# Kernel optimization log

Hardware: AMD Instinct MI355X
Metric: run time of the kernel (lower is better)

Reference implementation:

```python
import jax, jax.numpy as jnp
import numpy as np

K = 16  # neighbors


def _knn_indices(coords, k):
    # coords: (B, 3, N) -> indices (B, N, k) of k nearest points (incl. self)
    sq = jnp.sum(coords * coords, axis=1)                      # (B, N)
    d2 = sq[:, :, None] + sq[:, None, :] - 2.0 * jnp.einsum('bcn,bcm->bnm', coords, coords)
    _, idx = jax.lax.top_k(-d2, k)                             # smallest distances
    return idx


def _gather(points, idx):
    # points: (B, C, N), idx: (B, N, k) -> (B, C, N, k)
    return jax.vmap(lambda p, i: p[:, i])(points, idx)


def setup_inputs() -> dict:
    key = jax.random.key(0)
    ks = jax.random.split(key, 8)
    B, N, C_IN, C_OUT = 4, 8192, 64, 64
    s = 0.05
    return {
        'features': jax.random.normal(ks[0], (B, C_IN, N), dtype=jnp.float32),
        'coords': jax.random.normal(ks[1], (B, 3, N), dtype=jnp.float32),
        'w_lin': jax.random.normal(ks[2], (3 * C_OUT, C_IN), dtype=jnp.float32) * s,
        'w_theta1': jax.random.normal(ks[3], (C_OUT, 3), dtype=jnp.float32) * s,
        'w_theta2': jax.random.normal(ks[4], (C_OUT, C_OUT), dtype=jnp.float32) * s,
        'w_gamma1': jax.random.normal(ks[5], (C_OUT, C_OUT), dtype=jnp.float32) * s,
        'w_gamma2': jax.random.normal(ks[6], (C_OUT, C_OUT), dtype=jnp.float32) * s,
    }


def reference(features, coords, w_lin, w_theta1, w_theta2, w_gamma1, w_gamma2):
    # KNN (int indices, non-differentiable)
    idx = _knn_indices(coords, K)                              # (B, N, k)

    knn_coords = _gather(coords, idx)                          # (B, 3, N, k)
    rel = coords[:, :, :, None] - knn_coords                   # localize * -1
    delta = jnp.einsum('oc,bcnk->bonk', w_theta1, rel)
    delta = jax.nn.relu(jnp.einsum('oc,bcnk->bonk', w_theta2, delta))  # (B, Co, N, k)

    # input linear -> phi, psi, alpha
    feat3 = jnp.einsum('oc,bcn->bon', w_lin, features)         # (B, 3*Co, N)
    phi, psi, alpha = jnp.split(feat3, 3, axis=1)

    psi_g = _gather(psi, idx)                                  # (B, Co, N, k)
    inputs_gamma = phi[:, :, :, None] - psi_g + delta          # localize*-1 + delta
    g = jnp.einsum('oc,bcnk->bonk', w_gamma1, inputs_gamma)
    g = jax.nn.relu(jnp.einsum('oc,bcnk->bonk', w_gamma2, g))
    rho = jax.nn.softmax(g, axis=-1)                           # softmax over k

    alpha_g = _gather(alpha, idx) + delta                      # (B, Co, N, k)
    return jnp.sum(rho * alpha_g, axis=-1)                     # (B, Co, N)
```

## Files before the change

kernel.cpp:

```cpp
#include <hip/hip_runtime.h>
#include <cstdint>


#define NPT 8192
typedef unsigned long long u64;
typedef unsigned int u32;
typedef unsigned short u16;
typedef __attribute__((ext_vector_type(8))) short bf8_t;
typedef __attribute__((ext_vector_type(4))) float f32x4;

__device__ __forceinline__ u16 f2bf(float x) {
  return (u16)((__float_as_uint(x) + 0x8000u) >> 16);
}
__device__ __forceinline__ u32 pkbf(float lo, float hi) {
  return (u32)f2bf(lo) | ((u32)f2bf(hi) << 16);
}
__device__ __forceinline__ float bf2f(u16 v) {
  return __uint_as_float((u32)v << 16);
}
__device__ __forceinline__ u32 med3u(u32 a, u32 b, u32 c) {
  u32 d;
  asm("v_med3_u32 %0, %1, %2, %3" : "=v"(d) : "v"(a), "v"(b), "v"(c));
  return d;
}
__device__ __forceinline__ u32 wave_min_u32(u32 v) {
  u32 t;
  t = (u32)__builtin_amdgcn_update_dpp((int)v, (int)v, 0x111, 0xF, 0xF, false); v = min(v, t);
  t = (u32)__builtin_amdgcn_update_dpp((int)v, (int)v, 0x112, 0xF, 0xF, false); v = min(v, t);
  t = (u32)__builtin_amdgcn_update_dpp((int)v, (int)v, 0x114, 0xF, 0xF, false); v = min(v, t);
  t = (u32)__builtin_amdgcn_update_dpp((int)v, (int)v, 0x118, 0xF, 0xF, false); v = min(v, t);
  t = (u32)__builtin_amdgcn_update_dpp((int)v, (int)v, 0x142, 0xF, 0xF, false); v = min(v, t);
  t = (u32)__builtin_amdgcn_update_dpp((int)v, (int)v, 0x143, 0xF, 0xF, false); v = min(v, t);
  return (u32)__builtin_amdgcn_readlane((int)v, 63);
}
__device__ __forceinline__ u32 wave_max_u32(u32 v) {
  u32 t;
  t = (u32)__builtin_amdgcn_update_dpp((int)v, (int)v, 0x111, 0xF, 0xF, false); v = max(v, t);
  t = (u32)__builtin_amdgcn_update_dpp((int)v, (int)v, 0x112, 0xF, 0xF, false); v = max(v, t);
  t = (u32)__builtin_amdgcn_update_dpp((int)v, (int)v, 0x114, 0xF, 0xF, false); v = max(v, t);
  t = (u32)__builtin_amdgcn_update_dpp((int)v, (int)v, 0x118, 0xF, 0xF, false); v = max(v, t);
  t = (u32)__builtin_amdgcn_update_dpp((int)v, (int)v, 0x142, 0xF, 0xF, false); v = max(v, t);
  t = (u32)__builtin_amdgcn_update_dpp((int)v, (int)v, 0x143, 0xF, 0xF, false); v = max(v, t);
  return (u32)__builtin_amdgcn_readlane((int)v, 63);
}
__device__ __forceinline__ void lds_cp16(float4* lds_dst, const float4* gsrc) {
  __builtin_amdgcn_global_load_lds(
      (const __attribute__((address_space(1))) unsigned int*)(const void*)gsrc,
      (__attribute__((address_space(3))) unsigned int*)(void*)lds_dst, 16, 0, 0);
}

__global__ __launch_bounds__(256) void fold1_k(
    const float* __restrict__ wg1, const float* __restrict__ wg2,
    const float* __restrict__ wt1, const float* __restrict__ wt2,
    float* __restrict__ G, float* __restrict__ Mrow, float* __restrict__ McT) {
  int t = blockIdx.x * 256 + threadIdx.x;
  if (t < 4096) {
    int o = t >> 6, c = t & 63;
    float acc = 0.f;
    for (int cp = 0; cp < 64; ++cp) acc = fmaf(wg2[o * 64 + cp], wg1[cp * 64 + c], acc);
    G[o * 64 + c] = acc;
  } else if (t < 4096 + 192) {
    int i = t - 4096;
    int o = i / 3, j = i - o * 3;
    float acc = 0.f;
    for (int c = 0; c < 64; ++c) acc = fmaf(wt2[o * 64 + c], wt1[c * 3 + j], acc);
    Mrow[o * 3 + j] = acc;
    McT[j * 64 + o] = acc;
  }
}

__global__ __launch_bounds__(256) void fold2_k(
    const float* __restrict__ G, const float* __restrict__ wl,
    u16* __restrict__ GF, u16* __restrict__ WF) {
  int t = blockIdx.x * 256 + threadIdx.x;
  if (t < 12288) {
    int o = t >> 6, c = t & 63;
    float acc = 0.f;
    if (o < 64) {
      for (int cp = 0; cp < 64; ++cp) acc = fmaf(G[o * 64 + cp], wl[cp * 64 + c], acc);
    } else if (o < 128) {
      for (int cp = 0; cp < 64; ++cp) acc = fmaf(G[(o - 64) * 64 + cp], wl[(64 + cp) * 64 + c], acc);
    } else {
      acc = wl[o * 64 + c];
    }
    int ot = o >> 4, m = o & 15;
    int kh = c >> 5, q = (c >> 3) & 3, j = c & 7;
    WF[(((ot * 2 + kh) * 64) + (q * 16 + m)) * 8 + j] = f2bf(acc);
  } else {
    int i = t - 12288;
    int o = i >> 6, c = i & 63;
    int ot = o >> 4, m = o & 15;
    int kh = c >> 5, q = (c >> 3) & 3, j = c & 7;
    GF[(((ot * 2 + kh) * 64) + (q * 16 + m)) * 8 + j] = f2bf(G[o * 64 + c]);
  }
}

__global__ __launch_bounds__(256) void pack_k(const float* __restrict__ coords,
                                              float4* __restrict__ pack) {
  int g = blockIdx.x * 256 + threadIdx.x;
  int b = g >> 13, n = g & (NPT - 1);
  const float* c = coords + (size_t)b * 3 * NPT;
  float x = c[n], y = c[NPT + n], z = c[2 * NPT + n];
  float sq = __fadd_rn(__fadd_rn(__fmul_rn(x, x), __fmul_rn(y, y)), __fmul_rn(z, z));
  pack[g] = make_float4(x, y, z, sq);
}

#define QPB 8
#define CHUNK 1024
#define NQ 32768
__global__ __launch_bounds__(512) void knn_k(const float4* __restrict__ pack,
                                             u32* __restrict__ part) {
  __shared__ float4 C[2][CHUNK];
  int tid = threadIdx.x;
  int w = tid >> 6, lane = tid & 63;
  int query = blockIdx.x * QPB + w;
  int b = query >> 13, n = query & (NPT - 1);
  const float4* pk = pack + (size_t)b * NPT;
  float4 q = pk[n];
  float qsq = q.w;
  u32 arr[8];
#pragma unroll
  for (int j = 0; j < 8; ++j) arr[j] = 0xFFFFFFFFu;
  lds_cp16(&C[0][tid], pk + tid);
  lds_cp16(&C[0][512 + tid], pk + 512 + tid);
  __syncthreads();
  u32 tau = 0xFFFFFFFFu;
  for (int c0 = 0; c0 < NPT; c0 += CHUNK) {
    int cur = (c0 >> 10) & 1;
    if (c0 + CHUNK < NPT) {
      lds_cp16(&C[cur ^ 1][tid], pk + (c0 + CHUNK) + tid);
      lds_cp16(&C[cur ^ 1][512 + tid], pk + (c0 + CHUNK) + 512 + tid);
    }
#pragma unroll 4
    for (int t = 0; t < CHUNK / 64; ++t) {
      float4 c4 = C[cur][t * 64 + lane];
      float dot = fmaf(q.z, c4.z, fmaf(q.y, c4.y, q.x * c4.x));
      float d2 = fmaxf(fmaf(-2.f, dot, qsq + c4.w), 0.f);
      u32 key = (__float_as_uint(d2) & 0xFFFFE000u) | (u32)(c0 + t * 64 + lane);
      if (key < min(arr[7], tau)) {
        arr[7] = med3u(key, arr[6], arr[7]);
        arr[6] = med3u(key, arr[5], arr[6]);
        arr[5] = med3u(key, arr[4], arr[5]);
        arr[4] = med3u(key, arr[3], arr[4]);
        arr[3] = med3u(key, arr[2], arr[3]);
        arr[2] = med3u(key, arr[1], arr[2]);
        arr[1] = med3u(key, arr[0], arr[1]);
        arr[0] = min(arr[0], key);
      }
    }
    tau = wave_max_u32(arr[0]);
    __syncthreads();
  }
  u32 mg = 0xFFFFFFFFu;
#pragma unroll 1
  for (int r = 0; r < 24; ++r) {
    u32 m = wave_min_u32(arr[0]);
    if (lane == r) mg = m;
    if (arr[0] == m) {
      arr[0] = arr[1]; arr[1] = arr[2]; arr[2] = arr[3]; arr[3] = arr[4];
      arr[4] = arr[5]; arr[5] = arr[6]; arr[6] = arr[7]; arr[7] = 0xFFFFFFFFu;
    }
  }
  if (lane < 24) part[(size_t)lane * NQ + query] = mg;
}

__global__ __launch_bounds__(64) void refine_k(const float4* __restrict__ pack,
                                               const u32* __restrict__ part,
                                               int* __restrict__ idxk) {
  int g = blockIdx.x * 64 + threadIdx.x;
  int b = g >> 13;
  const float4* pk = pack + (size_t)b * NPT;
  float4 q = pk[g & (NPT - 1)];
  float qx = q.x, qy = q.y, qz = q.z, qs = q.w;
  float bd[16];
  int bi[16];
#pragma unroll
  for (int j = 0; j < 16; ++j) { bd[j] = 1e30f; bi[j] = 0x7FFFFFFF; }
#pragma unroll 4
  for (int j = 0; j < 24; ++j) {
    int m = (int)(part[(size_t)j * NQ + g] & 0x1FFFu);
    float4 pm = pk[m];
    float dot = __fadd_rn(__fadd_rn(__fmul_rn(qx, pm.x), __fmul_rn(qy, pm.y)),
                          __fmul_rn(qz, pm.z));
    float kd = __fsub_rn(__fadd_rn(qs, pm.w), __fmul_rn(2.0f, dot));
    int ki = m;
    if (kd < bd[15] || (kd == bd[15] && ki < bi[15])) {
#pragma unroll
      for (int qq = 0; qq < 16; ++qq) {
        bool cs = (kd < bd[qq]) || (kd == bd[qq] && ki < bi[qq]);
        float td = bd[qq];
        int ti = bi[qq];
        bd[qq] = cs ? kd : td;
        bi[qq] = cs ? ki : ti;
        kd = cs ? td : kd;
        ki = cs ? ti : ki;
      }
    }
  }
#pragma unroll
  for (int j = 0; j < 16; ++j) idxk[(size_t)g * 16 + j] = bi[j];
}

__global__ __launch_bounds__(256) void feat_k(const float* __restrict__ features,
                                              const u16* __restrict__ WF,
                                              float* __restrict__ featA,
                                              u16* __restrict__ featB) {
  int tid = threadIdx.x;
  int w = tid >> 6, l = tid & 63;
  int quad = l >> 4, col = l & 15;
  int P = blockIdx.x * 64 + w * 16 + col;
  int b = P >> 13, n = P & (NPT - 1);
  const float* fb = features + (size_t)b * 64 * NPT + n;
  const bf8_t* wfr = (const bf8_t*)WF;
  bf8_t Bf[2];
#pragma unroll
  for (int kh = 0; kh < 2; ++kh) {
    union { u32 wv[4]; bf8_t v; } ub;
#pragma unroll
    for (int j2 = 0; j2 < 4; ++j2) {
      float lo = fb[(size_t)(kh * 32 + quad * 8 + j2 * 2) * NPT];
      float hi = fb[(size_t)(kh * 32 + quad * 8 + j2 * 2 + 1) * NPT];
      ub.wv[j2] = pkbf(lo, hi);
    }
    Bf[kh] = ub.v;
  }
#pragma unroll
  for (int ot = 0; ot < 12; ++ot) {
    bf8_t A0 = wfr[(ot * 2 + 0) * 64 + l];
    bf8_t A1 = wfr[(ot * 2 + 1) * 64 + l];
    f32x4 acc = {0.f, 0.f, 0.f, 0.f};
    acc = __builtin_amdgcn_mfma_f32_16x16x32_bf16(A0, Bf[0], acc, 0, 0, 0);
    acc = __builtin_amdgcn_mfma_f32_16x16x32_bf16(A1, Bf[1], acc, 0, 0, 0);
    int gr = ot * 16 + quad * 4;
    if (ot < 4) {
      *(float4*)(featA + (size_t)P * 64 + gr) = make_float4(acc[0], acc[1], acc[2], acc[3]);
    } else {
      uint2 wv2 = make_uint2(pkbf(acc[0], acc[1]), pkbf(acc[2], acc[3]));
      *(uint2*)(featB + (size_t)P * 128 + (gr - 64)) = wv2;
    }
  }
}

#define SROW 68
__global__ __launch_bounds__(64) void attn_k(
    const float4* __restrict__ pack, const int* __restrict__ idxk,
    const float* __restrict__ featA, const u16* __restrict__ featB,
    const u16* __restrict__ GF, const float* __restrict__ Mrow,
    const float* __restrict__ McT, float* __restrict__ out) {
  __shared__ u16 S16[64 * SROW];
  int l = threadIdx.x;
  int quad = l >> 4, col = l & 15;
  int Pb = blockIdx.x * 4;
  int b = Pb >> 13;
  int nb0 = Pb & (NPT - 1);
  const float4* pkb = pack + (size_t)b * NPT;
  int idxv = idxk[(size_t)Pb * 16 + l];
  int mve[4];
#pragma unroll
  for (int t = 0; t < 4; ++t) mve[t] = __shfl(idxv, t * 16 + col);
  float relx[4], rely[4], relz[4];
#pragma unroll
  for (int t = 0; t < 4; ++t) {
    float4 own = pkb[nb0 + t];
    float4 nbr = pkb[mve[t]];
    relx[t] = own.x - nbr.x; rely[t] = own.y - nbr.y; relz[t] = own.z - nbr.z;
  }
  bf8_t Bf[4][2];
#pragma unroll
  for (int kh = 0; kh < 2; ++kh) {
    const float* mr = Mrow + (kh * 32 + quad * 8) * 3;
    float m_[24];
#pragma unroll
    for (int i6 = 0; i6 < 6; ++i6) {
      float4 v = *(const float4*)(mr + i6 * 4);
      m_[i6 * 4] = v.x; m_[i6 * 4 + 1] = v.y; m_[i6 * 4 + 2] = v.z; m_[i6 * 4 + 3] = v.w;
    }
#pragma unroll
    for (int t = 0; t < 4; ++t) {
      float u_[8];
#pragma unroll
      for (int j = 0; j < 8; ++j)
        u_[j] = fmaxf(fmaf(m_[j * 3 + 2], relz[t],
                           fmaf(m_[j * 3 + 1], rely[t], m_[j * 3] * relx[t])), 0.f);
      union { u32 w[4]; bf8_t v; } ub;
#pragma unroll
      for (int j2 = 0; j2 < 4; ++j2) ub.w[j2] = pkbf(u_[j2 * 2], u_[j2 * 2 + 1]);
      Bf[t][kh] = ub.v;
    }
  }
  const bf8_t* gfr = (const bf8_t*)GF;
#pragma unroll
  for (int ot = 0; ot < 4; ++ot) {
    bf8_t A0 = gfr[(ot * 2 + 0) * 64 + l];
    bf8_t A1 = gfr[(ot * 2 + 1) * 64 + l];
#pragma unroll
    for (int pt = 0; pt < 4; ++pt) {
      f32x4 acc = {0.f, 0.f, 0.f, 0.f};
      acc = __builtin_amdgcn_mfma_f32_16x16x32_bf16(A0, Bf[pt][0], acc, 0, 0, 0);
      acc = __builtin_amdgcn_mfma_f32_16x16x32_bf16(A1, Bf[pt][1], acc, 0, 0, 0);
      const float* phn = featA + (size_t)(Pb + pt) * 64 + ot * 16 + quad * 4;
      float4 ph = *(const float4*)phn;
      uint2 psw = *(const uint2*)(featB + ((size_t)b * NPT + mve[pt]) * 128 + ot * 16 + quad * 4);
      float g0 = fmaxf(acc[0] + ph.x - bf2f((u16)(psw.x & 0xFFFF)), 0.f);
      float g1 = fmaxf(acc[1] + ph.y - bf2f((u16)(psw.x >> 16)), 0.f);
      float g2 = fmaxf(acc[2] + ph.z - bf2f((u16)(psw.y & 0xFFFF)), 0.f);
      float g3 = fmaxf(acc[3] + ph.w - bf2f((u16)(psw.y >> 16)), 0.f);
      uint2 wv = make_uint2(pkbf(g0, g1), pkbf(g2, g3));
      *(uint2*)&S16[(pt * 16 + col) * SROW + ot * 16 + quad * 4] = wv;
    }
  }
  __syncthreads();
  float mc0 = McT[l], mc1 = McT[64 + l], mc2 = McT[128 + l];
  float accv[4];
#pragma unroll 1
  for (int pj = 0; pj < 4; ++pj) {
    float4 ownq = pkb[nb0 + pj];
    float gvv[16];
    float mx = -1e30f;
#pragma unroll
    for (int r = 0; r < 16; ++r) {
      gvv[r] = bf2f(S16[(pj * 16 + r) * SROW + l]);
      mx = fmaxf(mx, gvv[r]);
    }
    float s = 0.f;
#pragma unroll
    for (int r = 0; r < 16; ++r) {
      float e = __expf(gvv[r] - mx);
      gvv[r] = e;
      s += e;
    }
    float inv = 1.0f / s;
    float acc = 0.f;
#pragma unroll
    for (int r = 0; r < 16; ++r) {
      int si = __builtin_amdgcn_readlane(idxv, pj * 16 + r);
      float4 nbq = pkb[si];
      float dl = fmaxf(fmaf(mc2, ownq.z - nbq.z,
                            fmaf(mc1, ownq.y - nbq.y, mc0 * (ownq.x - nbq.x))), 0.f);
      float al = bf2f(featB[((size_t)b * NPT + si) * 128 + 64 + l]);
      acc = fmaf(gvv[r] * inv, al + dl, acc);
    }
    accv[pj] = acc;
  }
  *(float4*)(out + ((size_t)b * 64 + l) * NPT + nb0) =
      make_float4(accv[0], accv[1], accv[2], accv[3]);
}

extern "C" void kernel_launch(void* const* d_in, const int* in_sizes, int n_in,
                              void* d_out, int out_size, void* d_ws, size_t ws_size,
                              hipStream_t stream) {
  const float* features = (const float*)d_in[0];
  const float* coords = (const float*)d_in[1];
  const float* w_lin = (const float*)d_in[2];
  const float* w_t1 = (const float*)d_in[3];
  const float* w_t2 = (const float*)d_in[4];
  const float* w_g1 = (const float*)d_in[5];
  const float* w_g2 = (const float*)d_in[6];
  float* out = (float*)d_out;
  char* ws = (char*)d_ws;
  float4* pack = (float4*)ws;
  float* G = (float*)(ws + 524288);
  float* Mrow = (float*)(ws + 540672);
  float* McT = (float*)(ws + 541440);
  int* idxk = (int*)(ws + 591360);
  float* featA = (float*)(ws + 2688512);
  u16* featB = (u16*)(ws + 11077120);
  u32* part = (u32*)(ws + 2688512);
  u16* GF = (u16*)(ws + 19465728);
  u16* WF = (u16*)(ws + 19473920);

  fold1_k<<<17, 256, 0, stream>>>(w_g1, w_g2, w_t1, w_t2, G, Mrow, McT);
  fold2_k<<<64, 256, 0, stream>>>(G, w_lin, GF, WF);
  pack_k<<<128, 256, 0, stream>>>(coords, pack);
  knn_k<<<4096, 512, 0, stream>>>(pack, part);
  refine_k<<<512, 64, 0, stream>>>(pack, part, idxk);
  feat_k<<<512, 256, 0, stream>>>(features, WF, featA, featB);
  attn_k<<<8192, 64, 0, stream>>>(pack, idxk, featA, featB, GF, Mrow, McT, out);
}
```

Before: 294.2 us.

## Replace brute-force KNN scan with x-sorted bucketed search and early termination

Points are bucketed by x coordinate through a count, scan and scatter pipeline that yields an x-sorted copy with original indices and bin edges. Each query wave then scans outward left and right through the sorted array. It stops a direction once the x-gap squared exceeds the current wave-wide 8th-best threshold, so it no longer scans all 8192 candidates per query. This adds four small kernels, atomics and non-deterministic ordering within bins. Loads now come straight from global memory rather than an LDS-staged chunk, and the work per query depends on the data.

```diff
diff --git a/kernel.cpp b/kernel.cpp
--- a/kernel.cpp
+++ b/kernel.cpp
@@ -23,14 +23,18 @@
   asm("v_med3_u32 %0, %1, %2, %3" : "=v"(d) : "v"(a), "v"(b), "v"(c));
   return d;
 }
+__device__ __forceinline__ u32 umin2(u32 a, u32 b) { return a < b ? a : b; }
+__device__ __forceinline__ float rfl_f(float x) {
+  return __uint_as_float((u32)__builtin_amdgcn_readfirstlane((int)__float_as_uint(x)));
+}
 __device__ __forceinline__ u32 wave_min_u32(u32 v) {
   u32 t;
-  t = (u32)__builtin_amdgcn_update_dpp((int)v, (int)v, 0x111, 0xF, 0xF, false); v = min(v, t);
-  t = (u32)__builtin_amdgcn_update_dpp((int)v, (int)v, 0x112, 0xF, 0xF, false); v = min(v, t);
-  t = (u32)__builtin_amdgcn_update_dpp((int)v, (int)v, 0x114, 0xF, 0xF, false); v = min(v, t);
-  t = (u32)__builtin_amdgcn_update_dpp((int)v, (int)v, 0x118, 0xF, 0xF, false); v = min(v, t);
-  t = (u32)__builtin_amdgcn_update_dpp((int)v, (int)v, 0x142, 0xF, 0xF, false); v = min(v, t);
-  t = (u32)__builtin_amdgcn_update_dpp((int)v, (int)v, 0x143, 0xF, 0xF, false); v = min(v, t);
+  t = (u32)__builtin_amdgcn_update_dpp((int)v, (int)v, 0x111, 0xF, 0xF, false); v = umin2(v, t);
+  t = (u32)__builtin_amdgcn_update_dpp((int)v, (int)v, 0x112, 0xF, 0xF, false); v = umin2(v, t);
+  t = (u32)__builtin_amdgcn_update_dpp((int)v, (int)v, 0x114, 0xF, 0xF, false); v = umin2(v, t);
+  t = (u32)__builtin_amdgcn_update_dpp((int)v, (int)v, 0x118, 0xF, 0xF, false); v = umin2(v, t);
+  t = (u32)__builtin_amdgcn_update_dpp((int)v, (int)v, 0x142, 0xF, 0xF, false); v = umin2(v, t);
+  t = (u32)__builtin_amdgcn_update_dpp((int)v, (int)v, 0x143, 0xF, 0xF, false); v = umin2(v, t);
   return (u32)__builtin_amdgcn_readlane((int)v, 63);
 }
 __device__ __forceinline__ u32 wave_max_u32(u32 v) {
@@ -43,10 +47,15 @@
   t = (u32)__builtin_amdgcn_update_dpp((int)v, (int)v, 0x143, 0xF, 0xF, false); v = max(v, t);
   return (u32)__builtin_amdgcn_readlane((int)v, 63);
 }
-__device__ __forceinline__ void lds_cp16(float4* lds_dst, const float4* gsrc) {
-  __builtin_amdgcn_global_load_lds(
-      (const __attribute__((address_space(1))) unsigned int*)(const void*)gsrc,
-      (__attribute__((address_space(3))) unsigned int*)(void*)lds_dst, 16, 0, 0);
+__device__ __forceinline__ void ins8(u32* a, u32 key) {
+  a[7] = med3u(key, a[6], a[7]);
+  a[6] = med3u(key, a[5], a[6]);
+  a[5] = med3u(key, a[4], a[5]);
+  a[4] = med3u(key, a[3], a[4]);
+  a[3] = med3u(key, a[2], a[3]);
+  a[2] = med3u(key, a[1], a[2]);
+  a[1] = med3u(key, a[0], a[1]);
+  a[0] = umin2(a[0], key);
 }
 
 __global__ __launch_bounds__(256) void fold1_k(
@@ -105,52 +114,119 @@
   pack[g] = make_float4(x, y, z, sq);
 }
 
-#define QPB 8
-#define CHUNK 1024
+#define NB 1024
+#define XMIN -5.0f
+#define BW 0.009765625f
+#define INVBW 102.4f
 #define NQ 32768
-__global__ __launch_bounds__(512) void knn_k(const float4* __restrict__ pack,
+
+__global__ __launch_bounds__(1024) void zero_k(u32* __restrict__ cnt) {
+  cnt[blockIdx.x * 1024 + threadIdx.x] = 0;
+}
+
+__global__ __launch_bounds__(256) void cnt_k(const float4* __restrict__ pack,
+                                             u32* __restrict__ cnt) {
+  int g = blockIdx.x * 256 + threadIdx.x;
+  int b = g >> 13;
+  float x = pack[g].x;
+  int bi = (int)floorf((x - XMIN) * INVBW);
+  bi = bi < 0 ? 0 : (bi > NB - 1 ? NB - 1 : bi);
+  atomicAdd(&cnt[b * NB + bi], 1u);
+}
+
+__global__ __launch_bounds__(1024) void scan_k(const u32* __restrict__ cnt,
+                                               u32* __restrict__ cursor) {
+  __shared__ u32 S[NB];
+  int b = blockIdx.x, t = threadIdx.x;
+  u32 own = cnt[b * NB + t];
+  S[t] = own;
+  __syncthreads();
+  for (int off = 1; off < NB; off <<= 1) {
+    u32 v = (t >= off) ? S[t - off] : 0u;
+    __syncthreads();
+    S[t] += v;
+    __syncthreads();
+  }
+  cursor[b * NB + t] = S[t] - own;
+}
+
+__global__ __launch_bounds__(256) void scat_k(const float4* __restrict__ pack,
+                                              u32* __restrict__ cursor,
+                                              float4* __restrict__ spack,
+                                              int* __restrict__ sidx,
+                                              float* __restrict__ xedge) {
+  int g = blockIdx.x * 256 + threadIdx.x;
+  int b = g >> 13, n = g & (NPT - 1);
+  float4 p = pack[g];
+  int bi = (int)floorf((p.x - XMIN) * INVBW);
+  bi = bi < 0 ? 0 : (bi > NB - 1 ? NB - 1 : bi);
+  u32 pos = atomicAdd(&cursor[b * NB + bi], 1u);
+  size_t o = (size_t)b * NPT + pos;
+  spack[o] = p;
+  sidx[o] = n;
+  xedge[o] = fmaf((float)bi, BW, XMIN);
+}
+
+__global__ __launch_bounds__(256) void knn_k(const float4* __restrict__ spack,
+                                             const int* __restrict__ sidx,
+                                             const float* __restrict__ xedge,
                                              u32* __restrict__ part) {
-  __shared__ float4 C[2][CHUNK];
-  int tid = threadIdx.x;
-  int w = tid >> 6, lane = tid & 63;
-  int query = blockIdx.x * QPB + w;
-  int b = query >> 13, n = query & (NPT - 1);
-  const float4* pk = pack + (size_t)b * NPT;
-  float4 q = pk[n];
-  float qsq = q.w;
+  int gw = (blockIdx.x * 256 + threadIdx.x) >> 6;
+  int lane = threadIdx.x & 63;
+  int b = gw >> 13, c = gw & (NPT - 1);
+  const float4* sp = spack + (size_t)b * NPT;
+  const int* si = sidx + (size_t)b * NPT;
+  const float* xe = xedge + (size_t)b * NPT;
+  float4 qv = sp[c];
+  float qx = rfl_f(qv.x), qy = rfl_f(qv.y), qz = rfl_f(qv.z), qs = rfl_f(qv.w);
   u32 arr[8];
 #pragma unroll
   for (int j = 0; j < 8; ++j) arr[j] = 0xFFFFFFFFu;
-  lds_cp16(&C[0][tid], pk + tid);
-  lds_cp16(&C[0][512 + tid], pk + 512 + tid);
-  __syncthreads();
-  u32 tau = 0xFFFFFFFFu;
-  for (int c0 = 0; c0 < NPT; c0 += CHUNK) {
-    int cur = (c0 >> 10) & 1;
-    if (c0 + CHUNK < NPT) {
-      lds_cp16(&C[cur ^ 1][tid], pk + (c0 + CHUNK) + tid);
-      lds_cp16(&C[cur ^ 1][512 + tid], pk + (c0 + CHUNK) + 512 + tid);
-    }
-#pragma unroll 4
-    for (int t = 0; t < CHUNK / 64; ++t) {
-      float4 c4 = C[cur][t * 64 + lane];
-      float dot = fmaf(q.z, c4.z, fmaf(q.y, c4.y, q.x * c4.x));
-      float d2 = fmaxf(fmaf(-2.f, dot, qsq + c4.w), 0.f);
-      u32 key = (__float_as_uint(d2) & 0xFFFFE000u) | (u32)(c0 + t * 64 + lane);
-      if (key < min(arr[7], tau)) {
-        arr[7] = med3u(key, arr[6], arr[7]);
-        arr[6] = med3u(key, arr[5], arr[6]);
-        arr[5] = med3u(key, arr[4], arr[5]);
-        arr[4] = med3u(key, arr[3], arr[4]);
-        arr[3] = med3u(key, arr[2], arr[3]);
-        arr[2] = med3u(key, arr[1], arr[2]);
-        arr[1] = med3u(key, arr[0], arr[1]);
-        arr[0] = min(arr[0], key);
+  int R = c, L = c;
+  bool ra = true, la = (c > 0);
+#pragma unroll 1
+  while (ra || la) {
+    if (ra) {
+      int cand = R + lane;
+      bool ok = cand < NPT;
+      int cc = ok ? cand : NPT - 1;
+      float4 p = sp[cc];
+      u32 ki = (u32)si[cc];
+      float dot = fmaf(qz, p.z, fmaf(qy, p.y, qx * p.x));
+      float d2 = fmaxf(fmaf(-2.f, dot, qs + p.w), 0.f);
+      u32 key = ok ? ((__float_as_uint(d2) & 0xFFFFE000u) | ki) : 0xFFFFFFFFu;
+      ins8(arr, key);
+      R += 64;
+      if (R >= NPT) ra = false;
+    }
+    if (la) {
+      int base = L - 64;
+      int cand = base + lane;
+      bool ok = cand >= 0;
+      int cc = ok ? cand : 0;
+      float4 p = sp[cc];
+      u32 ki = (u32)si[cc];
+      float dot = fmaf(qz, p.z, fmaf(qy, p.y, qx * p.x));
+      float d2 = fmaxf(fmaf(-2.f, dot, qs + p.w), 0.f);
+      u32 key = ok ? ((__float_as_uint(d2) & 0xFFFFE000u) | ki) : 0xFFFFFFFFu;
+      ins8(arr, key);
+      L = base;
+      if (L <= 0) la = false;
+    }
+    u32 tau = wave_max_u32(arr[0]);
+    if (tau < 0xFF000000u) {
+      float tf = __uint_as_float((tau & 0xFFFFE000u) + 0x20000u);
+      if (ra) {
+        float dxr = (xe[R] - 1e-3f) - qx;
+        if (dxr > 0.f && dxr * dxr > tf) ra = false;
       }
-    }
-    tau = wave_max_u32(arr[0]);
-    __syncthreads();
-  }
+      if (la) {
+        float dxl = qx - (xe[L - 1] + (BW + 1e-3f));
+        if (dxl > 0.f && dxl * dxl > tf) la = false;
+      }
+    }
+  }
+  int qid = si[c];
   u32 mg = 0xFFFFFFFFu;
 #pragma unroll 1
   for (int r = 0; r < 24; ++r) {
@@ -161,7 +237,7 @@
       arr[4] = arr[5]; arr[5] = arr[6]; arr[6] = arr[7]; arr[7] = 0xFFFFFFFFu;
     }
   }
-  if (lane < 24) part[(size_t)lane * NQ + query] = mg;
+  if (lane < 24) part[(size_t)lane * NQ + (size_t)b * NPT + qid] = mg;
 }
 
 __global__ __launch_bounds__(64) void refine_k(const float4* __restrict__ pack,
@@ -334,9 +410,8 @@
 #pragma unroll
     for (int r = 0; r < 16; ++r) {
       int si = __builtin_amdgcn_readlane(idxv, pj * 16 + r);
-      float4 nbq = pkb[si];
-      float dl = fmaxf(fmaf(mc2, ownq.z - nbq.z,
-                            fmaf(mc1, ownq.y - nbq.y, mc0 * (ownq.x - nbq.x))), 0.f);
+      float dl = fmaxf(fmaf(mc2, ownq.z - pkb[si].z,
+                            fmaf(mc1, ownq.y - pkb[si].y, mc0 * (ownq.x - pkb[si].x))), 0.f);
       float al = bf2f(featB[((size_t)b * NPT + si) * 128 + 64 + l]);
       acc = fmaf(gvv[r] * inv, al + dl, acc);
     }
@@ -366,13 +441,22 @@
   float* featA = (float*)(ws + 2688512);
   u16* featB = (u16*)(ws + 11077120);
   u32* part = (u32*)(ws + 2688512);
+  float4* spack = (float4*)(ws + 11077120);
+  int* sidx = (int*)(ws + 11601408);
+  float* xedge = (float*)(ws + 11732480);
+  u32* cnt = (u32*)(ws + 11863552);
+  u32* cursor = (u32*)(ws + 11879936);
   u16* GF = (u16*)(ws + 19465728);
   u16* WF = (u16*)(ws + 19473920);
 
   fold1_k<<<17, 256, 0, stream>>>(w_g1, w_g2, w_t1, w_t2, G, Mrow, McT);
   fold2_k<<<64, 256, 0, stream>>>(G, w_lin, GF, WF);
   pack_k<<<128, 256, 0, stream>>>(coords, pack);
-  knn_k<<<4096, 512, 0, stream>>>(pack, part);
+  zero_k<<<4, 1024, 0, stream>>>(cnt);
+  cnt_k<<<128, 256, 0, stream>>>(pack, cnt);
+  scan_k<<<4, 1024, 0, stream>>>(cnt, cursor);
+  scat_k<<<128, 256, 0, stream>>>(pack, cursor, spack, sidx, xedge);
+  knn_k<<<8192, 256, 0, stream>>>(spack, sidx, xedge, part);
   refine_k<<<512, 64, 0, stream>>>(pack, part, idxk);
   feat_k<<<512, 256, 0, stream>>>(features, WF, featA, featB);
   attn_k<<<8192, 64, 0, stream>>>(pack, idxk, featA, featB, GF, Mrow, McT, out);
```

Measured after the change: 348.9 us. +18.6%, slower.
